# Performance work log

Measured on AMD Instinct MI355X. Metric: run time of the kernel, lower is better.

The kernel has to match this reference:

```python
import jax, jax.numpy as jnp
import numpy as np

N = 100000      # nodes
E = 1600000     # edges
IN_DIM = 500
HID = 64
OUT = 40
BN_EPS = 1e-5


def setup_inputs() -> dict:
    key = jax.random.key(0)
    ks = jax.random.split(key, 20)
    x = jax.random.normal(ks[0], (N, IN_DIM), dtype=jnp.float32)
    edge_index = jax.random.randint(ks[1], (2, E), 0, N, dtype=jnp.int64)

    def lin(k, fin, fout):
        return jax.random.normal(k, (fin, fout), dtype=jnp.float32) / np.sqrt(fin).astype(np.float32)

    inp = {
        "x": x,
        "edge_index": edge_index,
        "W1": lin(ks[2], IN_DIM, HID),
        "b1": jnp.zeros((HID,), jnp.float32),
        "g1": jnp.ones((HID,), jnp.float32),
        "be1": jnp.zeros((HID,), jnp.float32),
        "m1": 0.1 * jax.random.normal(ks[3], (HID,), jnp.float32),
        "v1": jax.random.uniform(ks[4], (HID,), jnp.float32, 0.5, 1.5),
        "W2": lin(ks[5], HID, HID),
        "b2": jnp.zeros((HID,), jnp.float32),
        "g2": jnp.ones((HID,), jnp.float32),
        "be2": jnp.zeros((HID,), jnp.float32),
        "m2": 0.1 * jax.random.normal(ks[6], (HID,), jnp.float32),
        "v2": jax.random.uniform(ks[7], (HID,), jnp.float32, 0.5, 1.5),
        "W3": lin(ks[8], HID, OUT),
        "b3": jnp.zeros((OUT,), jnp.float32),
    }
    return inp


def _gcn_conv(h, src, dst, deg_inv_sqrt, W, b):
    # PyG GCNConv (add_self_loops=True, normalize=True, eval math):
    # out = D^-1/2 (A + I) D^-1/2 (h @ W) + b
    h = h @ W                                    # [N, F]
    norm = deg_inv_sqrt[src] * deg_inv_sqrt[dst]  # [E]
    msg = h[src] * norm[:, None]                  # [E, F] gather
    agg = jax.ops.segment_sum(msg, dst, num_segments=N)  # scatter-add
    agg = agg + h * (deg_inv_sqrt * deg_inv_sqrt)[:, None]  # self-loop term
    return agg + b


def reference(x, edge_index, W1, b1, g1, be1, m1, v1,
              W2, b2, g2, be2, m2, v2, W3, b3):
    src, dst = edge_index[0], edge_index[1]
    # degree including self-loop
    deg = jax.ops.segment_sum(jnp.ones((E,), x.dtype), dst, num_segments=N) + 1.0
    deg_inv_sqrt = jax.lax.rsqrt(deg)

    def bn(h, g, be, m, v):
        return (h - m) * jax.lax.rsqrt(v + BN_EPS) * g + be

    h = _gcn_conv(x, src, dst, deg_inv_sqrt, W1, b1)
    h = jax.nn.relu(bn(h, g1, be1, m1, v1))
    # dropout: identity in eval mode
    h = _gcn_conv(h, src, dst, deg_inv_sqrt, W2, b2)
    h = jax.nn.relu(bn(h, g2, be2, m2, v2))
    out = _gcn_conv(h, src, dst, deg_inv_sqrt, W3, b3)
    return jax.nn.log_softmax(out, axis=1)
```

## Files before the change

kernel.cpp:

```cpp
#include <hip/hip_runtime.h>
#include <math.h>

#define N_NODES 100000
#define N_EDGES 1600000
#define IN_DIM  500
#define HID     64
#define OUT_DIM 40
#define BN_EPS  1e-5f
#define SCAN_NB 98
#define NTILE   6250

typedef _Float16 f16;
typedef __attribute__((ext_vector_type(2))) _Float16 f16x2;
typedef __attribute__((ext_vector_type(8))) _Float16 f16x8;
typedef __attribute__((ext_vector_type(4))) float f32x4;

static inline int cdiv(long a, int b) { return (int)((a + b - 1) / b); }

__device__ inline unsigned short f2h_bits(float f) {
    f16 h = (f16)f;
    return __builtin_bit_cast(unsigned short, h);
}
__device__ inline f16x2 bits2h2(unsigned int u) {
    return __builtin_bit_cast(f16x2, u);
}

__global__ void k_count_deg(const int* __restrict__ ei, int* degi) {
    int e = blockIdx.x * 256 + threadIdx.x;
    if (e < N_EDGES) atomicAdd(&degi[ei[N_EDGES + e]], 1);
}

__global__ void k_scan1(const int* __restrict__ degi, int* __restrict__ rowptr,
                        int* __restrict__ blocksum, float* __restrict__ dis) {
    __shared__ int sd[256];
    int tid = threadIdx.x;
    int base = blockIdx.x * 1024 + tid * 4;
    int v0 = (base + 0 < N_NODES) ? degi[base + 0] : -1;
    int v1 = (base + 1 < N_NODES) ? degi[base + 1] : -1;
    int v2 = (base + 2 < N_NODES) ? degi[base + 2] : -1;
    int v3 = (base + 3 < N_NODES) ? degi[base + 3] : -1;
    if (base + 0 < N_NODES) dis[base + 0] = rsqrtf((float)v0 + 1.0f);
    if (base + 1 < N_NODES) dis[base + 1] = rsqrtf((float)v1 + 1.0f);
    if (base + 2 < N_NODES) dis[base + 2] = rsqrtf((float)v2 + 1.0f);
    if (base + 3 < N_NODES) dis[base + 3] = rsqrtf((float)v3 + 1.0f);
    int w0 = v0 + 1, w1 = v1 + 1, w2 = v2 + 1, w3 = v3 + 1;
    int s = w0 + w1 + w2 + w3;
    sd[tid] = s;
    __syncthreads();
    for (int off = 1; off < 256; off <<= 1) {
        int t = (tid >= off) ? sd[tid - off] : 0;
        __syncthreads();
        sd[tid] += t;
        __syncthreads();
    }
    int excl = sd[tid] - s;
    if (base + 0 < N_NODES) rowptr[base + 0] = excl;
    if (base + 1 < N_NODES) rowptr[base + 1] = excl + w0;
    if (base + 2 < N_NODES) rowptr[base + 2] = excl + w0 + w1;
    if (base + 3 < N_NODES) rowptr[base + 3] = excl + w0 + w1 + w2;
    if (tid == 255) blocksum[blockIdx.x] = sd[255];
}

__global__ void k_scan2(int* __restrict__ blocksum, int* __restrict__ blockbase) {
    __shared__ int sd[128];
    int tid = threadIdx.x;
    int v = (tid < SCAN_NB) ? blocksum[tid] : 0;
    sd[tid] = v;
    __syncthreads();
    for (int off = 1; off < 128; off <<= 1) {
        int t = (tid >= off) ? sd[tid - off] : 0;
        __syncthreads();
        sd[tid] += t;
        __syncthreads();
    }
    if (tid < SCAN_NB) blockbase[tid] = sd[tid] - v;
}

__global__ void k_scan3(int* __restrict__ rowptr, const int* __restrict__ blockbase,
                        const int* __restrict__ degi, int* __restrict__ cursor,
                        uint2* __restrict__ epack) {
    int add = blockbase[blockIdx.x];
    int base = blockIdx.x * 1024 + threadIdx.x * 4;
#pragma unroll
    for (int i = 0; i < 4; ++i) {
        int node = base + i;
        if (node < N_NODES) {
            int rp = rowptr[node] + add;
            rowptr[node] = rp;
            float d2 = 1.0f / (float)(degi[node] + 1);
            unsigned int hb = f2h_bits(d2);
            epack[rp] = make_uint2((unsigned int)(node * 128), (hb << 16) | hb);
            cursor[node] = 1;
        }
    }
    if (blockIdx.x == 0 && threadIdx.x == 0)
        rowptr[N_NODES] = N_EDGES + N_NODES;
}

__global__ void k_permute(const int* __restrict__ ei, const int* __restrict__ rowptr,
                          int* __restrict__ cursor, const float* __restrict__ dis,
                          uint2* __restrict__ epack) {
    int e = blockIdx.x * 256 + threadIdx.x;
    if (e >= N_EDGES) return;
    int s = ei[e];
    int d = ei[N_EDGES + e];
    int pos = rowptr[d] + atomicAdd(&cursor[d], 1);
    unsigned int hb = f2h_bits(dis[s] * dis[d]);
    epack[pos] = make_uint2((unsigned int)(s * 128), (hb << 16) | hb);
}

__device__ inline void convW_one(const float* W, unsigned short* wb,
                                 int idx, int K, int F) {
    int j    = idx & 7;
    int lane = (idx >> 3) & 63;
    int q    = idx >> 9;
    int t    = q >> 2, nt = q & 3;
    int n = nt * 16 + (lane & 15);
    int k = t * 32 + ((lane >> 4) << 3) + j;
    float v = (k < K && n < F) ? W[(long)k * F + n] : 0.f;
    wb[idx] = f2h_bits(v);
}

__global__ void k_convall(const float* __restrict__ W1, const float* __restrict__ W2,
                          const float* __restrict__ W3,
                          unsigned short* __restrict__ wb1,
                          unsigned short* __restrict__ wb2,
                          unsigned short* __restrict__ wb3) {
    int idx = blockIdx.x * 256 + threadIdx.x;
    if (idx < 32768) {
        convW_one(W1, wb1, idx, IN_DIM, HID);
    } else if (idx < 36864) {
        convW_one(W2, wb2, idx - 32768, HID, HID);
    } else {
        convW_one(W3, wb3, idx - 36864, HID, OUT_DIM);
    }
}

__global__ void k_bnfold(const float* __restrict__ b1, const float* __restrict__ g1,
                         const float* __restrict__ be1, const float* __restrict__ m1,
                         const float* __restrict__ v1,
                         const float* __restrict__ b2, const float* __restrict__ g2,
                         const float* __restrict__ be2, const float* __restrict__ m2,
                         const float* __restrict__ v2,
                         unsigned short* __restrict__ sc1,
                         unsigned short* __restrict__ sc2) {
    int t = threadIdx.x;
    int c = t & 63;
    const float *b, *g, *be, *m, *v;
    unsigned short* sc;
    if (t < 64) { b = b1; g = g1; be = be1; m = m1; v = v1; sc = sc1; }
    else        { b = b2; g = g2; be = be2; m = m2; v = v2; sc = sc2; }
    float S = g[c] * rsqrtf(v[c] + BN_EPS);
    float C = (b[c] - m[c]) * S + be[c];
    sc[c]      = f2h_bits(S);
    sc[64 + c] = f2h_bits(C);
}

__global__ __launch_bounds__(256) void k_l1fused(
        const float* __restrict__ x,
        const unsigned short* __restrict__ wb,
        unsigned short* __restrict__ h) {
    __shared__ unsigned short l[16 * 520];
    const int rt = blockIdx.x;
    const int tid = threadIdx.x;

#pragma unroll
    for (int it = 0; it < 8; ++it) {
        int slot = it * 256 + tid;
        int row = slot >> 7, kq = slot & 127;
        float4 v = make_float4(0.f, 0.f, 0.f, 0.f);
        if (kq < 125)
            v = *reinterpret_cast<const float4*>(x + ((long)rt * 16 + row) * IN_DIM + kq * 4);
        unsigned int u0 = (unsigned int)f2h_bits(v.x) | ((unsigned int)f2h_bits(v.y) << 16);
        unsigned int u1 = (unsigned int)f2h_bits(v.z) | ((unsigned int)f2h_bits(v.w) << 16);
        *reinterpret_cast<uint2*>(&l[row * 520 + kq * 4]) = make_uint2(u0, u1);
    }
    __syncthreads();

    const int wid  = tid >> 6;
    const int lane = tid & 63;
    const int l15  = lane & 15;
    const int lhi  = lane >> 4;

    const f16x8* bp = reinterpret_cast<const f16x8*>(wb) + wid * 64 + lane;
    const unsigned short* arow = &l[l15 * 520 + lhi * 8];

    f32x4 acc = (f32x4){0.f, 0.f, 0.f, 0.f};
    f16x8 ca = *reinterpret_cast<const f16x8*>(arow);
    f16x8 cb = bp[0];

#pragma unroll
    for (int t = 0; t < 16; ++t) {
        f16x8 na, nb;
        if (t < 15) {
            na = *reinterpret_cast<const f16x8*>(arow + (t + 1) * 32);
            nb = bp[(t + 1) * 256];
        }
        acc = __builtin_amdgcn_mfma_f32_16x16x32_f16(ca, cb, acc, 0, 0, 0);
        if (t < 15) { ca = na; cb = nb; }
    }

#pragma unroll
    for (int rr = 0; rr < 4; ++rr) {
        long grow = (long)rt * 16 + lhi * 4 + rr;
        h[grow * 64 + wid * 16 + l15] = f2h_bits(acc[rr]);
    }
}

template <int T>
__global__ __launch_bounds__(256) void k_gemm_packed(
        const unsigned short* __restrict__ xp,
        const unsigned short* __restrict__ wb,
        unsigned short* __restrict__ h) {
    const int tid  = threadIdx.x;
    const int wid  = tid >> 6;
    const int lane = tid & 63;
    const int rt   = blockIdx.x * 4 + wid;
    if (rt >= NTILE) return;

    const f16x8* ap = reinterpret_cast<const f16x8*>(xp) + (long)rt * T * 64 + lane;
    const f16x8* bp = reinterpret_cast<const f16x8*>(wb) + lane;

    f32x4 acc[4];
#pragma unroll
    for (int nt = 0; nt < 4; ++nt) acc[nt] = (f32x4){0.f, 0.f, 0.f, 0.f};

    f16x8 ca = ap[0];
    f16x8 cb0 = bp[0], cb1 = bp[64], cb2 = bp[128], cb3 = bp[192];

    for (int t = 0; t < T; ++t) {
        f16x8 na, nb0, nb1, nb2, nb3;
        if (t + 1 < T) {
            na  = ap[(t + 1) * 64];
            nb0 = bp[((t + 1) * 4 + 0) * 64];
            nb1 = bp[((t + 1) * 4 + 1) * 64];
            nb2 = bp[((t + 1) * 4 + 2) * 64];
            nb3 = bp[((t + 1) * 4 + 3) * 64];
        }
        acc[0] = __builtin_amdgcn_mfma_f32_16x16x32_f16(ca, cb0, acc[0], 0, 0, 0);
        acc[1] = __builtin_amdgcn_mfma_f32_16x16x32_f16(ca, cb1, acc[1], 0, 0, 0);
        acc[2] = __builtin_amdgcn_mfma_f32_16x16x32_f16(ca, cb2, acc[2], 0, 0, 0);
        acc[3] = __builtin_amdgcn_mfma_f32_16x16x32_f16(ca, cb3, acc[3], 0, 0, 0);
        if (t + 1 < T) { ca = na; cb0 = nb0; cb1 = nb1; cb2 = nb2; cb3 = nb3; }
    }

    const int l15 = lane & 15, lhi = lane >> 4;
#pragma unroll
    for (int nt = 0; nt < 4; ++nt) {
        int coln = nt * 16 + l15;
#pragma unroll
        for (int rr = 0; rr < 4; ++rr) {
            long grow = (long)rt * 16 + lhi * 4 + rr;
            h[grow * 64 + coln] = f2h_bits(acc[nt][rr]);
        }
    }
}

__global__ __launch_bounds__(256) void k_agg_bn_relu(
        const unsigned short* __restrict__ h, const int* __restrict__ rowptr,
        const uint2* __restrict__ epack, const unsigned short* __restrict__ sc,
        unsigned short* __restrict__ xp_out) {
    int node = blockIdx.x * 4 + (threadIdx.x >> 6);
    if (node >= N_NODES) return;
    const int lane = threadIdx.x & 63;
    const int e8 = lane >> 3, c8 = lane & 7;

    const int start = rowptr[node];
    const int cnt   = rowptr[node + 1] - start;
    const uint2* ep = epack + start;
    const char*  hb = (const char*)h + c8 * 16;

    f16x2 a[4] = {(f16x2)0, (f16x2)0, (f16x2)0, (f16x2)0};

    auto batch = [&](int j) {
        int jj = j + e8;
        bool valid = jj < cnt;
        uint2 mv = ep[valid ? jj : 0];
        f16x2 w2 = bits2h2(valid ? mv.y : 0u);
        uint4 hv = *(const uint4*)(hb + mv.x);
        a[0] += bits2h2(hv.x) * w2;
        a[1] += bits2h2(hv.y) * w2;
        a[2] += bits2h2(hv.z) * w2;
        a[3] += bits2h2(hv.w) * w2;
    };

    int j = 0;
    for (; j + 8 < cnt; j += 16) { batch(j); batch(j + 8); }
    if (j < cnt) batch(j);

#pragma unroll
    for (int off = 8; off < 64; off <<= 1) {
#pragma unroll
        for (int i = 0; i < 4; ++i) {
            unsigned int u = __builtin_bit_cast(unsigned int, a[i]);
            a[i] += bits2h2((unsigned int)__shfl_xor((int)u, off));
        }
    }

    if (e8 == 0) {
        uint4 Su = *(const uint4*)(sc + c8 * 8);
        uint4 Cu = *(const uint4*)(sc + 64 + c8 * 8);
        unsigned int sw[4] = {Su.x, Su.y, Su.z, Su.w};
        unsigned int cw[4] = {Cu.x, Cu.y, Cu.z, Cu.w};
        unsigned int u[4];
#pragma unroll
        for (int p = 0; p < 4; ++p) {
            f16x2 r = a[p] * bits2h2(sw[p]) + bits2h2(cw[p]);
            r[0] = r[0] > (f16)0 ? r[0] : (f16)0;
            r[1] = r[1] > (f16)0 ? r[1] : (f16)0;
            u[p] = __builtin_bit_cast(unsigned int, r);
        }

        int n16 = node & 15, rt2 = node >> 4;
        long base = (((long)rt2 * 2 + (c8 >> 2)) * 64 + (c8 & 3) * 16 + n16) * 8;
        *reinterpret_cast<uint4*>(xp_out + base) = make_uint4(u[0], u[1], u[2], u[3]);
    }
}

__global__ __launch_bounds__(256) void k_agg_lsm(
        const unsigned short* __restrict__ h, const int* __restrict__ rowptr,
        const uint2* __restrict__ epack,
        const float* __restrict__ bias, float* __restrict__ out) {
    int node = blockIdx.x * 4 + (threadIdx.x >> 6);
    if (node >= N_NODES) return;
    const int lane = threadIdx.x & 63;
    const int e8 = lane >> 3, c8 = lane & 7;

    const int start = rowptr[node];
    const int cnt   = rowptr[node + 1] - start;
    const uint2* ep = epack + start;
    const char*  hb = (const char*)h + c8 * 16;

    f16x2 a[4] = {(f16x2)0, (f16x2)0, (f16x2)0, (f16x2)0};

    auto batch = [&](int j) {
        int jj = j + e8;
        bool valid = jj < cnt;
        uint2 mv = ep[valid ? jj : 0];
        f16x2 w2 = bits2h2(valid ? mv.y : 0u);
        uint4 hv = *(const uint4*)(hb + mv.x);
        a[0] += bits2h2(hv.x) * w2;
        a[1] += bits2h2(hv.y) * w2;
        a[2] += bits2h2(hv.z) * w2;
        a[3] += bits2h2(hv.w) * w2;
    };

    int j = 0;
    for (; j + 8 < cnt; j += 16) { batch(j); batch(j + 8); }
    if (j < cnt) batch(j);

#pragma unroll
    for (int off = 8; off < 64; off <<= 1) {
#pragma unroll
        for (int i = 0; i < 4; ++i) {
            unsigned int u = __builtin_bit_cast(unsigned int, a[i]);
            a[i] += bits2h2((unsigned int)__shfl_xor((int)u, off));
        }
    }

    const bool ok = c8 < 5;
    float av[8] = {(float)a[0][0], (float)a[0][1], (float)a[1][0], (float)a[1][1],
                   (float)a[2][0], (float)a[2][1], (float)a[3][0], (float)a[3][1]};
    float vals[8];
    float mx = -INFINITY;
    if (ok) {
        float4 bb0 = *(const float4*)(bias + c8 * 8), bb1 = *(const float4*)(bias + c8 * 8 + 4);
        float bbv[8] = {bb0.x, bb0.y, bb0.z, bb0.w, bb1.x, bb1.y, bb1.z, bb1.w};
#pragma unroll
        for (int i = 0; i < 8; ++i) {
            vals[i] = av[i] + bbv[i];
            mx = fmaxf(mx, vals[i]);
        }
    }
#pragma unroll
    for (int o = 1; o < 8; o <<= 1) mx = fmaxf(mx, __shfl_xor(mx, o));
    float es = 0.f;
    if (ok) {
#pragma unroll
        for (int i = 0; i < 8; ++i) es += expf(vals[i] - mx);
    }
#pragma unroll
    for (int o = 1; o < 8; o <<= 1) es += __shfl_xor(es, o);
    float ls = logf(es);

    if (e8 == 0 && ok) {
        float* op = out + (long)node * 40 + c8 * 8;
        *(float4*)op = make_float4(vals[0] - mx - ls, vals[1] - mx - ls,
                                   vals[2] - mx - ls, vals[3] - mx - ls);
        *(float4*)(op + 4) = make_float4(vals[4] - mx - ls, vals[5] - mx - ls,
                                         vals[6] - mx - ls, vals[7] - mx - ls);
    }
}

extern "C" void kernel_launch(void* const* d_in, const int* in_sizes, int n_in,
                              void* d_out, int out_size, void* d_ws, size_t ws_size,
                              hipStream_t stream) {
    const float* x   = (const float*)d_in[0];
    const int*   ei  = (const int*)d_in[1];
    const float* W1  = (const float*)d_in[2];
    const float* b1  = (const float*)d_in[3];
    const float* g1  = (const float*)d_in[4];
    const float* be1 = (const float*)d_in[5];
    const float* m1  = (const float*)d_in[6];
    const float* v1  = (const float*)d_in[7];
    const float* W2  = (const float*)d_in[8];
    const float* b2  = (const float*)d_in[9];
    const float* g2  = (const float*)d_in[10];
    const float* be2 = (const float*)d_in[11];
    const float* m2  = (const float*)d_in[12];
    const float* v2  = (const float*)d_in[13];
    const float* W3  = (const float*)d_in[14];
    const float* b3  = (const float*)d_in[15];
    float* out = (float*)d_out;

    float* ws        = (float*)d_ws;
    float* dis       = ws;
    int*   degi      = (int*)(ws + 100096);
    int*   cursor    = (int*)(ws + 200192);
    int*   rowptr    = (int*)(ws + 300288);
    int*   blocksum  = (int*)(ws + 400384);
    int*   blockbase = (int*)(ws + 400512);
    uint2* epack     = (uint2*)(ws + 400640);
    unsigned short* bufH = (unsigned short*)(ws + 3800640);
    unsigned short* xp2  = (unsigned short*)(ws + 32400640);
    unsigned short* xp3  = (unsigned short*)(ws + 35600640);
    unsigned short* wb1  = (unsigned short*)(ws + 38800640);
    unsigned short* wb2  = (unsigned short*)(ws + 38817024);
    unsigned short* wb3  = (unsigned short*)(ws + 38819072);
    unsigned short* sc1  = (unsigned short*)(ws + 38821120);
    unsigned short* sc2  = sc1 + 128;

    hipMemsetAsync(degi, 0, 100096 * sizeof(int), stream);
    k_count_deg<<<cdiv(N_EDGES, 256), 256, 0, stream>>>(ei, degi);
    k_scan1<<<SCAN_NB, 256, 0, stream>>>(degi, rowptr, blocksum, dis);
    k_scan2<<<1, 128, 0, stream>>>(blocksum, blockbase);
    k_scan3<<<SCAN_NB, 256, 0, stream>>>(rowptr, blockbase, degi, cursor, epack);
    k_permute<<<cdiv(N_EDGES, 256), 256, 0, stream>>>(ei, rowptr, cursor, dis, epack);

    k_convall<<<160, 256, 0, stream>>>(W1, W2, W3, wb1, wb2, wb3);
    k_bnfold<<<1, 128, 0, stream>>>(b1, g1, be1, m1, v1, b2, g2, be2, m2, v2, sc1, sc2);

    const int gemm_grid = cdiv(NTILE, 4);
    const int agg_grid  = cdiv(N_NODES, 4);

    k_l1fused<<<NTILE, 256, 0, stream>>>(x, wb1, bufH);
    k_agg_bn_relu<<<agg_grid, 256, 0, stream>>>(bufH, rowptr, epack, sc1, xp2);

    k_gemm_packed<2><<<gemm_grid, 256, 0, stream>>>(xp2, wb2, bufH);
    k_agg_bn_relu<<<agg_grid, 256, 0, stream>>>(bufH, rowptr, epack, sc2, xp3);

    k_gemm_packed<2><<<gemm_grid, 256, 0, stream>>>(xp3, wb3, bufH);
    k_agg_lsm<<<agg_grid, 256, 0, stream>>>(bufH, rowptr, epack, b3, out);
}
```

Baseline: 363.1 us.

## Fuse aggregation+BN+ReLU with following GEMM via shared-memory tile

Merges the per-node aggregation/BN/ReLU kernel with the next layer's 64-wide MFMA GEMM. Each block aggregates 16 nodes (4 per wave), stages the activated rows in LDS, then runs the GEMM from LDS, and writes to separate ping-pong buffers. This removes the global round-trip of the packed intermediate and two kernel launches. In exchange, each wave now handles four nodes one after another, which lowers parallelism in the gather phase and adds a block-wide barrier.

```diff
diff --git a/kernel.cpp b/kernel.cpp
--- a/kernel.cpp
+++ b/kernel.cpp
@@ -207,113 +207,87 @@
     }
 }
 
-template <int T>
-__global__ __launch_bounds__(256) void k_gemm_packed(
-        const unsigned short* __restrict__ xp,
-        const unsigned short* __restrict__ wb,
-        unsigned short* __restrict__ h) {
+__global__ __launch_bounds__(256) void k_agg_gemm(
+        const unsigned short* __restrict__ h_in, const int* __restrict__ rowptr,
+        const uint2* __restrict__ epack, const unsigned short* __restrict__ sc,
+        const unsigned short* __restrict__ wb, unsigned short* __restrict__ h_out) {
+    __shared__ unsigned short st[16 * 80];
+    const int base = blockIdx.x * 16;
     const int tid  = threadIdx.x;
     const int wid  = tid >> 6;
     const int lane = tid & 63;
-    const int rt   = blockIdx.x * 4 + wid;
-    if (rt >= NTILE) return;
-
-    const f16x8* ap = reinterpret_cast<const f16x8*>(xp) + (long)rt * T * 64 + lane;
-    const f16x8* bp = reinterpret_cast<const f16x8*>(wb) + lane;
-
-    f32x4 acc[4];
-#pragma unroll
-    for (int nt = 0; nt < 4; ++nt) acc[nt] = (f32x4){0.f, 0.f, 0.f, 0.f};
-
-    f16x8 ca = ap[0];
-    f16x8 cb0 = bp[0], cb1 = bp[64], cb2 = bp[128], cb3 = bp[192];
-
-    for (int t = 0; t < T; ++t) {
-        f16x8 na, nb0, nb1, nb2, nb3;
-        if (t + 1 < T) {
-            na  = ap[(t + 1) * 64];
-            nb0 = bp[((t + 1) * 4 + 0) * 64];
-            nb1 = bp[((t + 1) * 4 + 1) * 64];
-            nb2 = bp[((t + 1) * 4 + 2) * 64];
-            nb3 = bp[((t + 1) * 4 + 3) * 64];
-        }
-        acc[0] = __builtin_amdgcn_mfma_f32_16x16x32_f16(ca, cb0, acc[0], 0, 0, 0);
-        acc[1] = __builtin_amdgcn_mfma_f32_16x16x32_f16(ca, cb1, acc[1], 0, 0, 0);
-        acc[2] = __builtin_amdgcn_mfma_f32_16x16x32_f16(ca, cb2, acc[2], 0, 0, 0);
-        acc[3] = __builtin_amdgcn_mfma_f32_16x16x32_f16(ca, cb3, acc[3], 0, 0, 0);
-        if (t + 1 < T) { ca = na; cb0 = nb0; cb1 = nb1; cb2 = nb2; cb3 = nb3; }
-    }
+    const int e8 = lane >> 3, c8 = lane & 7;
+
+    for (int sub = 0; sub < 4; ++sub) {
+        const int node  = base + wid * 4 + sub;
+        const int start = rowptr[node];
+        const int cnt   = rowptr[node + 1] - start;
+        const uint2* ep = epack + start;
+        const char*  hb = (const char*)h_in + c8 * 16;
+
+        f16x2 a[4] = {(f16x2)0, (f16x2)0, (f16x2)0, (f16x2)0};
+
+        auto batch = [&](int j) {
+            int jj = j + e8;
+            bool valid = jj < cnt;
+            uint2 mv = ep[valid ? jj : 0];
+            f16x2 w2 = bits2h2(valid ? mv.y : 0u);
+            uint4 hv = *(const uint4*)(hb + mv.x);
+            a[0] += bits2h2(hv.x) * w2;
+            a[1] += bits2h2(hv.y) * w2;
+            a[2] += bits2h2(hv.z) * w2;
+            a[3] += bits2h2(hv.w) * w2;
+        };
+
+        int j = 0;
+        for (; j + 8 < cnt; j += 16) { batch(j); batch(j + 8); }
+        if (j < cnt) batch(j);
+
+#pragma unroll
+        for (int off = 8; off < 64; off <<= 1) {
+#pragma unroll
+            for (int i = 0; i < 4; ++i) {
+                unsigned int u = __builtin_bit_cast(unsigned int, a[i]);
+                a[i] += bits2h2((unsigned int)__shfl_xor((int)u, off));
+            }
+        }
+
+        if (e8 == 0) {
+            uint4 Su = *(const uint4*)(sc + c8 * 8);
+            uint4 Cu = *(const uint4*)(sc + 64 + c8 * 8);
+            unsigned int sw[4] = {Su.x, Su.y, Su.z, Su.w};
+            unsigned int cw[4] = {Cu.x, Cu.y, Cu.z, Cu.w};
+            unsigned int u[4];
+#pragma unroll
+            for (int p = 0; p < 4; ++p) {
+                f16x2 r = a[p] * bits2h2(sw[p]) + bits2h2(cw[p]);
+                r[0] = r[0] > (f16)0 ? r[0] : (f16)0;
+                r[1] = r[1] > (f16)0 ? r[1] : (f16)0;
+                u[p] = __builtin_bit_cast(unsigned int, r);
+            }
+            int row = wid * 4 + sub;
+            *reinterpret_cast<uint4*>(&st[row * 80 + c8 * 8]) =
+                make_uint4(u[0], u[1], u[2], u[3]);
+        }
+    }
+    __syncthreads();
 
     const int l15 = lane & 15, lhi = lane >> 4;
-#pragma unroll
-    for (int nt = 0; nt < 4; ++nt) {
-        int coln = nt * 16 + l15;
-#pragma unroll
-        for (int rr = 0; rr < 4; ++rr) {
-            long grow = (long)rt * 16 + lhi * 4 + rr;
-            h[grow * 64 + coln] = f2h_bits(acc[nt][rr]);
-        }
-    }
-}
-
-__global__ __launch_bounds__(256) void k_agg_bn_relu(
-        const unsigned short* __restrict__ h, const int* __restrict__ rowptr,
-        const uint2* __restrict__ epack, const unsigned short* __restrict__ sc,
-        unsigned short* __restrict__ xp_out) {
-    int node = blockIdx.x * 4 + (threadIdx.x >> 6);
-    if (node >= N_NODES) return;
-    const int lane = threadIdx.x & 63;
-    const int e8 = lane >> 3, c8 = lane & 7;
-
-    const int start = rowptr[node];
-    const int cnt   = rowptr[node + 1] - start;
-    const uint2* ep = epack + start;
-    const char*  hb = (const char*)h + c8 * 16;
-
-    f16x2 a[4] = {(f16x2)0, (f16x2)0, (f16x2)0, (f16x2)0};
-
-    auto batch = [&](int j) {
-        int jj = j + e8;
-        bool valid = jj < cnt;
-        uint2 mv = ep[valid ? jj : 0];
-        f16x2 w2 = bits2h2(valid ? mv.y : 0u);
-        uint4 hv = *(const uint4*)(hb + mv.x);
-        a[0] += bits2h2(hv.x) * w2;
-        a[1] += bits2h2(hv.y) * w2;
-        a[2] += bits2h2(hv.z) * w2;
-        a[3] += bits2h2(hv.w) * w2;
-    };
-
-    int j = 0;
-    for (; j + 8 < cnt; j += 16) { batch(j); batch(j + 8); }
-    if (j < cnt) batch(j);
-
-#pragma unroll
-    for (int off = 8; off < 64; off <<= 1) {
-#pragma unroll
-        for (int i = 0; i < 4; ++i) {
-            unsigned int u = __builtin_bit_cast(unsigned int, a[i]);
-            a[i] += bits2h2((unsigned int)__shfl_xor((int)u, off));
-        }
-    }
-
-    if (e8 == 0) {
-        uint4 Su = *(const uint4*)(sc + c8 * 8);
-        uint4 Cu = *(const uint4*)(sc + 64 + c8 * 8);
-        unsigned int sw[4] = {Su.x, Su.y, Su.z, Su.w};
-        unsigned int cw[4] = {Cu.x, Cu.y, Cu.z, Cu.w};
-        unsigned int u[4];
-#pragma unroll
-        for (int p = 0; p < 4; ++p) {
-            f16x2 r = a[p] * bits2h2(sw[p]) + bits2h2(cw[p]);
-            r[0] = r[0] > (f16)0 ? r[0] : (f16)0;
-            r[1] = r[1] > (f16)0 ? r[1] : (f16)0;
-            u[p] = __builtin_bit_cast(unsigned int, r);
-        }
-
-        int n16 = node & 15, rt2 = node >> 4;
-        long base = (((long)rt2 * 2 + (c8 >> 2)) * 64 + (c8 & 3) * 16 + n16) * 8;
-        *reinterpret_cast<uint4*>(xp_out + base) = make_uint4(u[0], u[1], u[2], u[3]);
+    const unsigned short* arow = &st[l15 * 80 + lhi * 8];
+    const f16x8* bp = reinterpret_cast<const f16x8*>(wb) + wid * 64 + lane;
+
+    f32x4 acc = (f32x4){0.f, 0.f, 0.f, 0.f};
+    f16x8 a0 = *reinterpret_cast<const f16x8*>(arow);
+    f16x8 a1 = *reinterpret_cast<const f16x8*>(arow + 32);
+    f16x8 b0 = bp[0];
+    f16x8 b1 = bp[256];
+    acc = __builtin_amdgcn_mfma_f32_16x16x32_f16(a0, b0, acc, 0, 0, 0);
+    acc = __builtin_amdgcn_mfma_f32_16x16x32_f16(a1, b1, acc, 0, 0, 0);
+
+#pragma unroll
+    for (int rr = 0; rr < 4; ++rr) {
+        long grow = (long)base + lhi * 4 + rr;
+        h_out[grow * 64 + wid * 16 + l15] = f2h_bits(acc[rr]);
     }
 }
 
@@ -421,14 +395,14 @@
     int*   blocksum  = (int*)(ws + 400384);
     int*   blockbase = (int*)(ws + 400512);
     uint2* epack     = (uint2*)(ws + 400640);
-    unsigned short* bufH = (unsigned short*)(ws + 3800640);
-    unsigned short* xp2  = (unsigned short*)(ws + 32400640);
-    unsigned short* xp3  = (unsigned short*)(ws + 35600640);
-    unsigned short* wb1  = (unsigned short*)(ws + 38800640);
-    unsigned short* wb2  = (unsigned short*)(ws + 38817024);
-    unsigned short* wb3  = (unsigned short*)(ws + 38819072);
-    unsigned short* sc1  = (unsigned short*)(ws + 38821120);
-    unsigned short* sc2  = sc1 + 128;
+    unsigned short* h1 = (unsigned short*)(ws + 3800640);
+    unsigned short* h2 = (unsigned short*)(ws + 7000640);
+    unsigned short* h3 = (unsigned short*)(ws + 10200640);
+    unsigned short* wb1 = (unsigned short*)(ws + 13400640);
+    unsigned short* wb2 = (unsigned short*)(ws + 13417024);
+    unsigned short* wb3 = (unsigned short*)(ws + 13419072);
+    unsigned short* sc1 = (unsigned short*)(ws + 13421120);
+    unsigned short* sc2 = sc1 + 128;
 
     hipMemsetAsync(degi, 0, 100096 * sizeof(int), stream);
     k_count_deg<<<cdiv(N_EDGES, 256), 256, 0, stream>>>(ei, degi);
@@ -440,15 +414,13 @@
     k_convall<<<160, 256, 0, stream>>>(W1, W2, W3, wb1, wb2, wb3);
     k_bnfold<<<1, 128, 0, stream>>>(b1, g1, be1, m1, v1, b2, g2, be2, m2, v2, sc1, sc2);
 
-    const int gemm_grid = cdiv(NTILE, 4);
-    const int agg_grid  = cdiv(N_NODES, 4);
-
-    k_l1fused<<<NTILE, 256, 0, stream>>>(x, wb1, bufH);
-    k_agg_bn_relu<<<agg_grid, 256, 0, stream>>>(bufH, rowptr, epack, sc1, xp2);
-
-    k_gemm_packed<2><<<gemm_grid, 256, 0, stream>>>(xp2, wb2, bufH);
-    k_agg_bn_relu<<<agg_grid, 256, 0, stream>>>(bufH, rowptr, epack, sc2, xp3);
-
-    k_gemm_packed<2><<<gemm_grid, 256, 0, stream>>>(xp3, wb3, bufH);
-    k_agg_lsm<<<agg_grid, 256, 0, stream>>>(bufH, rowptr, epack, b3, out);
-}
+    const int agg_grid = cdiv(N_NODES, 4);
+
+    k_l1fused<<<NTILE, 256, 0, stream>>>(x, wb1, h1);
+
+    k_agg_gemm<<<NTILE, 256, 0, stream>>>(h1, rowptr, epack, sc1, wb2, h2);
+
+    k_agg_gemm<<<NTILE, 256, 0, stream>>>(h2, rowptr, epack, sc2, wb3, h3);
+
+    k_agg_lsm<<<agg_grid, 256, 0, stream>>>(h3, rowptr, epack, b3, out);
+}
```

Measured after the change: 343.8 us. -5.3%, faster.
